# Performance work log

Measured on AMD Instinct MI355X. Metric: run time of the kernel, lower is better.

The kernel has to match this reference:

```python
import jax, jax.numpy as jnp
import numpy as np

KERNEL_SIZE = 9  # square structuring element, matches __init__ default
ITERATIONS = 1


def setup_inputs() -> dict:
    key = jax.random.key(0)
    label = jax.random.uniform(key, (16, 1024, 1024, 1), dtype=jnp.float32)
    return {"label": label}


def reference(label):
    # cv2.dilate with np.ones((k,k)) == sliding-window max over a k x k square.
    # Default morphology border value for dilate is -inf, so SAME padding with
    # -inf init reproduces cv2's border behavior exactly.
    out = label
    for _ in range(ITERATIONS):
        out = jax.lax.reduce_window(
            out,
            -jnp.inf,
            jax.lax.max,
            window_dimensions=(1, KERNEL_SIZE, KERNEL_SIZE, 1),
            window_strides=(1, 1, 1, 1),
            padding="SAME",
        )
    # Original layer wraps the result in K.stop_gradient.
    return jax.lax.stop_gradient(out)
```

## Files before the change

kernel.cpp:

```cpp
#include <hip/hip_runtime.h>
#include <math.h>

#define IMG  1024
#define ROWS 32

#define NEG4 make_float4(-INFINITY, -INFINITY, -INFINITY, -INFINITY)

__device__ __forceinline__ float4 max4(const float4 a, const float4 b) {
    return make_float4(fmaxf(a.x, b.x), fmaxf(a.y, b.y),
                       fmaxf(a.z, b.z), fmaxf(a.w, b.w));
}

__global__ __launch_bounds__(256, 1)
void dilate9x9(const float* __restrict__ in, float* __restrict__ out) {
    const int tid  = threadIdx.x;
    const int lane = tid & 63;
    const int x0   = tid << 2;
    const int y0   = blockIdx.x * ROWS;
    const int b    = blockIdx.y;

    const float* img  = in  + (size_t)b * IMG * IMG;
    float*       oimg = out + (size_t)b * IMG * IMG;

    const bool eL = (lane == 0)  && (x0 > 0);
    const bool eR = (lane == 63) && (x0 < IMG - 4);
    const int  xe = eL ? (x0 - 4) : (x0 + 4);

    auto hmax_row = [&](const float4 v, const float4 e) -> float4 {
        const float pre1 = fmaxf(v.x, v.y);
        const float pre2 = fmaxf(pre1, v.z);
        const float pre3 = fmaxf(pre2, v.w);
        const float suf2 = fmaxf(v.z, v.w);
        const float suf1 = fmaxf(v.y, suf2);
        const float suf0 = fmaxf(v.x, suf1);
        float ps0 = __shfl_up(suf0, 1, 64);
        float ps1 = __shfl_up(suf1, 1, 64);
        float ps2 = __shfl_up(suf2, 1, 64);
        float ps3 = __shfl_up(v.w , 1, 64);
        float np0 = __shfl_down(v.x , 1, 64);
        float np1 = __shfl_down(pre1, 1, 64);
        float np2 = __shfl_down(pre2, 1, 64);
        float np3 = __shfl_down(pre3, 1, 64);
        if (lane == 0) {
            ps3 = e.w;
            ps2 = fmaxf(e.z, e.w);
            ps1 = fmaxf(e.y, ps2);
            ps0 = fmaxf(e.x, ps1);
        }
        if (lane == 63) {
            np0 = e.x;
            np1 = fmaxf(e.x, e.y);
            np2 = fmaxf(np1, e.z);
            np3 = fmaxf(np2, e.w);
        }
        float4 r;
        r.x = fmaxf(fmaxf(ps0, suf0), np0);
        r.y = fmaxf(fmaxf(ps1, suf0), np1);
        r.z = fmaxf(fmaxf(ps2, suf0), np2);
        r.w = fmaxf(fmaxf(ps3, suf0), np3);
        return r;
    };

    auto load8 = [&](float4 (&V)[8], float4 (&E)[8], const int iyBase, const bool clampHi) {
        #pragma unroll
        for (int j = 0; j < 8; ++j) {
            const int iy = iyBase + j;
            const int cy = clampHi ? (iy < IMG ? iy : IMG - 1) : (iy >= 0 ? iy : 0);
            const size_t ro = (size_t)cy * IMG;
            V[j] = *reinterpret_cast<const float4*>(img + ro + x0);
            E[j] = NEG4;
            if (eL | eR) E[j] = *reinterpret_cast<const float4*>(img + ro + xe);
        }
    };

    float4 C[8];
    float4 V0[8], E0[8], V1[8], E1[8];

    load8(V0, E0, y0 - 4, false);
    #pragma unroll
    for (int j = 0; j < 8; ++j)
        C[j] = (y0 - 4 + j >= 0) ? hmax_row(V0[j], E0[j]) : NEG4;

    load8(V0, E0, y0 + 4, true);

    auto chunk = [&](const int c, float4 (&Vc)[8], float4 (&Ec)[8],
                     float4 (&Vn)[8], float4 (&En)[8]) {
        const int r0 = y0 + (c << 3);
        if (c < (ROWS / 8) - 1) load8(Vn, En, r0 + 12, true);

        float4 S[8];
        S[7] = C[7];
        #pragma unroll
        for (int j = 6; j >= 0; --j) S[j] = max4(C[j], S[j + 1]);

        float4 P;
        #pragma unroll
        for (int t = 0; t < 8; ++t) {
            const float4 H = (r0 + 4 + t < IMG) ? hmax_row(Vc[t], Ec[t]) : NEG4;
            P = (t == 0) ? H : max4(P, H);
            *reinterpret_cast<float4*>(oimg + (size_t)(r0 + t) * IMG + x0) = max4(S[t], P);
            C[t] = H;
        }
    };

    chunk(0, V0, E0, V1, E1);
    chunk(1, V1, E1, V0, E0);
    chunk(2, V0, E0, V1, E1);
    chunk(3, V1, E1, V0, E0);
}

extern "C" void kernel_launch(void* const* d_in, const int* in_sizes, int n_in,
                              void* d_out, int out_size, void* d_ws, size_t ws_size,
                              hipStream_t stream) {
    const float* in  = (const float*)d_in[0];
    float*       out = (float*)d_out;
    const int B = in_sizes[0] / (IMG * IMG);
    dim3 grid(IMG / ROWS, B);
    dilate9x9<<<grid, 256, 0, stream>>>(in, out);
}
```

Measured before the change: 28.97 us.

## Replace chunked van Herk vertical max with rolling 9-row window and 4-deep prefetch

Replaces the 8-row double-buffered load chunks and prefix/suffix vertical max with a rolling ring of 9 horizontal-max rows. Each output row is now a direct 8-op max over the ring, and the next input row is prefetched 4 rows ahead, with sched_barrier pinning the issue order. This cuts register use for the prefetch buffers and gives a steady per-row load/compute stream. The cost is more vertical max operations per output row (8 instead of about 2-3) and tighter control over scheduling, which may limit how far the compiler can hide memory latency.

After: 29.02 us. No clear change (+0.2%).

```diff
diff --git a/kernel.cpp b/kernel.cpp
--- a/kernel.cpp
+++ b/kernel.cpp
@@ -15,16 +15,24 @@
 void dilate9x9(const float* __restrict__ in, float* __restrict__ out) {
     const int tid  = threadIdx.x;
     const int lane = tid & 63;
-    const int x0   = tid << 2;
+    const int x4   = tid << 2;
     const int y0   = blockIdx.x * ROWS;
     const int b    = blockIdx.y;
 
     const float* img  = in  + (size_t)b * IMG * IMG;
     float*       oimg = out + (size_t)b * IMG * IMG;
 
-    const bool eL = (lane == 0)  && (x0 > 0);
-    const bool eR = (lane == 63) && (x0 < IMG - 4);
-    const int  xe = eL ? (x0 - 4) : (x0 + 4);
+    const bool eL = (lane == 0)  && (x4 > 0);
+    const bool eR = (lane == 63) && (x4 < IMG - 4);
+    const int  xe = eL ? (x4 - 4) : (x4 + 4);
+
+    auto ldrow = [&](const int iy, float4& V, float4& E) {
+        const int cy = iy < 0 ? 0 : (iy >= IMG ? IMG - 1 : iy);
+        const size_t ro = (size_t)cy * IMG;
+        V = *reinterpret_cast<const float4*>(img + ro + x4);
+        E = NEG4;
+        if (eL | eR) E = *reinterpret_cast<const float4*>(img + ro + xe);
+    };
 
     auto hmax_row = [&](const float4 v, const float4 e) -> float4 {
         const float pre1 = fmaxf(v.x, v.y);
@@ -61,52 +69,40 @@
         return r;
     };
 
-    auto load8 = [&](float4 (&V)[8], float4 (&E)[8], const int iyBase, const bool clampHi) {
-        #pragma unroll
-        for (int j = 0; j < 8; ++j) {
-            const int iy = iyBase + j;
-            const int cy = clampHi ? (iy < IMG ? iy : IMG - 1) : (iy >= 0 ? iy : 0);
-            const size_t ro = (size_t)cy * IMG;
-            V[j] = *reinterpret_cast<const float4*>(img + ro + x0);
-            E[j] = NEG4;
-            if (eL | eR) E[j] = *reinterpret_cast<const float4*>(img + ro + xe);
-        }
-    };
+    float4 H[9];
+    float4 Vr[4], Er[4];
 
-    float4 C[8];
-    float4 V0[8], E0[8], V1[8], E1[8];
+    float4 PV[8], PE[8];
+    #pragma unroll
+    for (int j = 0; j < 8; ++j) ldrow(y0 - 4 + j, PV[j], PE[j]);
+    #pragma unroll
+    for (int d = 0; d < 4; ++d) ldrow(y0 + 4 + d, Vr[d], Er[d]);
+    __builtin_amdgcn_sched_barrier(0);
 
-    load8(V0, E0, y0 - 4, false);
     #pragma unroll
     for (int j = 0; j < 8; ++j)
-        C[j] = (y0 - 4 + j >= 0) ? hmax_row(V0[j], E0[j]) : NEG4;
+        H[j] = (y0 - 4 + j >= 0) ? hmax_row(PV[j], PE[j]) : NEG4;
 
-    load8(V0, E0, y0 + 4, true);
+    #pragma unroll
+    for (int r = 0; r < ROWS; ++r) {
+        const bool valid = (y0 + r + 4 < IMG);
+        H[(r + 8) % 9] = valid ? hmax_row(Vr[r & 3], Er[r & 3]) : NEG4;
 
-    auto chunk = [&](const int c, float4 (&Vc)[8], float4 (&Ec)[8],
-                     float4 (&Vn)[8], float4 (&En)[8]) {
-        const int r0 = y0 + (c << 3);
-        if (c < (ROWS / 8) - 1) load8(Vn, En, r0 + 12, true);
+        if (r < ROWS - 4) {
+            ldrow(y0 + r + 8, Vr[r & 3], Er[r & 3]);
+            __builtin_amdgcn_sched_barrier(0);
+        }
 
-        float4 S[8];
-        S[7] = C[7];
-        #pragma unroll
-        for (int j = 6; j >= 0; --j) S[j] = max4(C[j], S[j + 1]);
-
-        float4 P;
-        #pragma unroll
-        for (int t = 0; t < 8; ++t) {
-            const float4 H = (r0 + 4 + t < IMG) ? hmax_row(Vc[t], Ec[t]) : NEG4;
-            P = (t == 0) ? H : max4(P, H);
-            *reinterpret_cast<float4*>(oimg + (size_t)(r0 + t) * IMG + x0) = max4(S[t], P);
-            C[t] = H;
-        }
-    };
-
-    chunk(0, V0, E0, V1, E1);
-    chunk(1, V1, E1, V0, E0);
-    chunk(2, V0, E0, V1, E1);
-    chunk(3, V1, E1, V0, E0);
+        float4 o = max4(H[0], H[1]);
+        o = max4(o, H[2]);
+        o = max4(o, H[3]);
+        o = max4(o, H[4]);
+        o = max4(o, H[5]);
+        o = max4(o, H[6]);
+        o = max4(o, H[7]);
+        o = max4(o, H[8]);
+        *reinterpret_cast<float4*>(oimg + (size_t)(y0 + r) * IMG + x4) = o;
+    }
 }
 
 extern "C" void kernel_launch(void* const* d_in, const int* in_sizes, int n_in,
```
